# Kernel tuning notes

Measured on AMD Instinct MI355X. Metric: run time of the kernel, lower is better.

The kernel has to match this reference:

```python
import jax, jax.numpy as jnp
import numpy as np

# Core Cutie memory read: L2 affinity with shrinkage/selection + softmax + value readout.
# similarity(n,p) = (-sum_c mk_c(n)^2 * qe_c(p) + 2*sum_c mk_c(n)*qk_c(p)*qe_c(p)
#                   - sum_c qe_c(p)*qk_c(p)^2) * ms(n) / sqrt(CK)
# affinity = softmax over memory dim n; readout = value @ affinity.

NUM_OBJECTS = 3
VALUE_DIM = 512
KEY_DIM = 64
T_MEM, H16, W16 = 16, 30, 54  # 16 memory frames, stride-16 features of 480x864


def setup_inputs() -> dict:
    k = jax.random.key(0)
    k0, k1, k2, k3, k4 = jax.random.split(k, 5)
    B = 1
    N = T_MEM * H16 * W16
    return {
        "memory_key": jax.random.normal(k0, (B, KEY_DIM, N), jnp.float32),
        "memory_shrinkage": jax.random.uniform(k1, (B, 1, N), jnp.float32),
        "key": jax.random.normal(k2, (B, KEY_DIM, H16, W16), jnp.float32),
        "selection": jax.random.uniform(k3, (B, KEY_DIM, H16, W16), jnp.float32),
        "memory_mask_value": jax.random.normal(k4, (B, NUM_OBJECTS, VALUE_DIM, N), jnp.float32),
    }


def reference(memory_key, memory_shrinkage, key, selection, memory_mask_value):
    B, O, CV, N = memory_mask_value.shape
    Ck = memory_key.shape[1]
    H, W = key.shape[-2:]
    P = H * W
    qk = key.reshape(B, Ck, P)        # query keys,      b c p
    qe = selection.reshape(B, Ck, P)  # query selection, b c p
    mk = memory_key                   # memory keys,     b c n
    # anisotropic squared-L2 similarity (XMem/Cutie), shape b n p
    a_sq = jnp.einsum("bcn,bcp->bnp", mk * mk, qe)
    two_ab = 2.0 * jnp.einsum("bcn,bcp->bnp", mk, qk * qe)
    b_sq = jnp.sum(qe * qk * qk, axis=1, keepdims=True)  # b 1 p
    sim = (-a_sq + two_ab - b_sq) * memory_shrinkage[:, 0, :, None]
    sim = sim / jnp.sqrt(jnp.asarray(Ck, sim.dtype))
    affinity = jax.nn.softmax(sim, axis=1)  # softmax over memory elements n
    value = memory_mask_value.reshape(B, O * CV, N)
    mem = jnp.einsum("bvn,bnp->bvp", value, affinity)  # weighted readout
    return mem.reshape(B, O, CV, H, W)
```

## Files before the change

### kernel.cpp

```cpp
#include <hip/hip_runtime.h>
#include <hip/hip_bf16.h>


#define NTOT 25920
#define PTOT 1620
#define VTOT 1536
#define PPAD 1664
#define PPAD2 1792
#define NPAD 25984
#define KF   128
#define SPLITS 6

typedef __hip_bfloat16 bf16;
using frag  = __attribute__((ext_vector_type(8))) short;
using f32x4 = __attribute__((ext_vector_type(4))) float;

#define GLOBAL_AS __attribute__((address_space(1)))
#define LDS_AS    __attribute__((address_space(3)))
__device__ __forceinline__ void async_copy16(void* l, const void* g) {
    __builtin_amdgcn_global_load_lds((const GLOBAL_AS void*)g, (LDS_AS void*)l,
                                     16, 0, 0);
}

#define OFF_FLAG ((size_t)0)
#define OFF_QF   ((size_t)64)
#define OFF_NF   ((size_t)426048)
#define OFF_BSQ  ((size_t)7077952)
#define OFF_MSC  ((size_t)7084608)
#define OFF_SUM  ((size_t)7188544)
#define OFF_ACC  ((size_t)7195200)
#define OFF_ES   ((size_t)17148480)
#define OFF_VALB ((size_t)110045760)
#define NEED_BIG ((size_t)189672000)
#define OFF_PART ((size_t)189672000)
#define NEED_PART ((size_t)249391680)

__global__ void detect_dtype(const unsigned short* __restrict__ mk16,
                             unsigned* __restrict__ flag) {
    int i = threadIdx.x;
    unsigned e = (mk16[2 * i] >> 7) & 0xFFu;
    unsigned long long bad = __ballot(e >= 0x8Fu);
    if (i == 0) *flag = bad ? 1u : 0u;
}

__device__ __forceinline__ float load_in(const void* p, int idx, bool f32) {
    return f32 ? ((const float*)p)[idx]
               : __bfloat162float(((const bf16*)p)[idx]);
}

__global__ __launch_bounds__(256) void prep_q(const void* __restrict__ key,
                                              const void* __restrict__ sel,
                                              bf16* __restrict__ qf,
                                              float* __restrict__ bsq,
                                              float* __restrict__ sums,
                                              const unsigned* __restrict__ flag) {
    const bool f32 = (*flag != 0u);
    int p = blockIdx.x * 256 + threadIdx.x;
    if (p >= PPAD) return;
    float acc = 0.f;
    for (int c = 0; c < 64; ++c) {
        float qk = 0.f, qe = 0.f;
        if (p < PTOT) {
            qk = load_in(key, c * PTOT + p, f32);
            qe = load_in(sel, c * PTOT + p, f32);
        }
        qf[p * KF + c]      = __float2bfloat16(-qe);
        qf[p * KF + 64 + c] = __float2bfloat16(2.f * qk * qe);
        acc += qe * qk * qk;
    }
    bsq[p]  = acc;
    sums[p] = 0.f;
}

__global__ __launch_bounds__(256) void prep_n(const void* __restrict__ mkey,
                                              const void* __restrict__ shr,
                                              bf16* __restrict__ nf,
                                              float* __restrict__ msc,
                                              const unsigned* __restrict__ flag) {
    const bool f32 = (*flag != 0u);
    int n = blockIdx.x * 256 + threadIdx.x;
    if (n >= NPAD) return;
    for (int c = 0; c < 64; ++c) {
        float mk = (n < NTOT) ? load_in(mkey, c * NTOT + n, f32) : 0.f;
        nf[n * KF + c]      = __float2bfloat16(mk * mk);
        nf[n * KF + 64 + c] = __float2bfloat16(mk);
    }
    msc[n] = (n < NTOT) ? load_in(shr, n, f32) * 0.125f : 0.f;
}

__global__ __launch_bounds__(256) void conv_val(const void* __restrict__ val,
                                                bf16* __restrict__ valb,
                                                const unsigned* __restrict__ flag) {
    const bool f32 = (*flag != 0u);
    size_t base = ((size_t)blockIdx.x * 256 + threadIdx.x) * 8;
    if (base >= (size_t)VTOT * NTOT) return;
    if (f32) {
        const float4 v0 = *(const float4*)((const float*)val + base);
        const float4 v1 = *(const float4*)((const float*)val + base + 4);
        bf16 o[8] = {__float2bfloat16(v0.x), __float2bfloat16(v0.y),
                     __float2bfloat16(v0.z), __float2bfloat16(v0.w),
                     __float2bfloat16(v1.x), __float2bfloat16(v1.y),
                     __float2bfloat16(v1.z), __float2bfloat16(v1.w)};
        *(uint4*)(valb + base) = *(const uint4*)o;
    } else {
        *(uint4*)(valb + base) = *(const uint4*)((const bf16*)val + base);
    }
}

#define EST_LD 136
__global__ __launch_bounds__(256) void sim_kernel(const bf16* __restrict__ qf,
                                                  const bf16* __restrict__ nf,
                                                  const float* __restrict__ bsq,
                                                  const float* __restrict__ msc,
                                                  float* __restrict__ sums,
                                                  bf16* __restrict__ es) {
    __shared__ __align__(16) char smem[65536];
    short* As  = (short*)smem;
    short* Bs  = (short*)(smem + 32768);
    short* Est = (short*)smem;

    const int tid = threadIdx.x;
    const int nt = blockIdx.x, pt = blockIdx.y;
    const int p0 = pt * 128, n0 = nt * 128;
    const int w = tid >> 6, lane = tid & 63;

    for (int it = 0; it < 8; ++it) {
        int rb = it * 16 + w * 4;
        int r  = rb + (lane >> 4);
        int cg = (lane & 15) ^ (r & 15);
        async_copy16(&As[rb * KF], qf + (size_t)(p0 + r) * KF + cg * 8);
    }
    for (int it = 0; it < 8; ++it) {
        int rb = it * 16 + w * 4;
        int r  = rb + (lane >> 4);
        int cg = (lane & 15) ^ (r & 15);
        async_copy16(&Bs[rb * KF], nf + (size_t)(n0 + r) * KF + cg * 8);
    }
    __syncthreads();

    const int low = lane & 15, quad = lane >> 4;
    const int wr = w >> 1, wc = w & 1;

    f32x4 acc[4][4] = {};
    for (int kk = 0; kk < 4; ++kk) {
        frag a[4], b[4];
        for (int i = 0; i < 4; ++i) {
            int row = wr * 64 + i * 16 + low;
            a[i] = *(const frag*)&As[row * KF + (((kk * 4 + quad) ^ low) * 8)];
        }
        for (int j = 0; j < 4; ++j) {
            int row = wc * 64 + j * 16 + low;
            b[j] = *(const frag*)&Bs[row * KF + (((kk * 4 + quad) ^ low) * 8)];
        }
        for (int i = 0; i < 4; ++i)
            for (int j = 0; j < 4; ++j)
                acc[i][j] = __builtin_amdgcn_mfma_f32_16x16x32_bf16(a[i], b[j], acc[i][j], 0, 0, 0);
    }

    float msv[4];
    for (int j = 0; j < 4; ++j) msv[j] = msc[n0 + wc * 64 + j * 16 + low];
    __syncthreads();

    for (int i = 0; i < 4; ++i) {
        const int prow = p0 + wr * 64 + i * 16 + quad * 4;
        const float4 bq = *(const float4*)(bsq + prow);
        const float bs[4] = {bq.x, bq.y, bq.z, bq.w};
        for (int r = 0; r < 4; ++r) {
            const int p = prow + r;
            const int rloc = wr * 64 + i * 16 + quad * 4 + r;
            float vsum = 0.f;
            for (int j = 0; j < 4; ++j) {
                const int n = n0 + wc * 64 + j * 16 + low;
                float e = 0.f;
                if (n < NTOT) e = __expf((acc[i][j][r] - bs[r]) * msv[j]);
                vsum += e;
                Est[rloc * EST_LD + wc * 64 + j * 16 + low] = __bfloat16_as_short(__float2bfloat16(e));
            }
            vsum += __shfl_xor(vsum, 1);
            vsum += __shfl_xor(vsum, 2);
            vsum += __shfl_xor(vsum, 4);
            vsum += __shfl_xor(vsum, 8);
            if (p < PTOT && low == 0) atomicAdd(&sums[p], vsum);
        }
    }
    __syncthreads();

    const int row = tid >> 1, half = tid & 1;
    const int p = p0 + row;
    if (p < PTOT) {
        bf16* dst = es + (size_t)p * NTOT + n0 + half * 64;
        const short* src = Est + row * EST_LD + half * 64;
        for (int m = 0; m < 8; ++m) {
            int ng = n0 + half * 64 + m * 8;
            if (ng + 8 <= NTOT)
                *(uint4*)(dst + m * 8) = *(const uint4*)(src + m * 8);
        }
    }
}

__global__ __launch_bounds__(512) void gemm_big(const bf16* __restrict__ val,
                                                const bf16* __restrict__ es,
                                                const float* __restrict__ sums,
                                                float* __restrict__ out,
                                                float* __restrict__ part,
                                                int use_part) {
    __shared__ __align__(16) short As[3][2][128 * 64];
    __shared__ __align__(16) short Bs[2][2][128 * 64];
    const int tid = threadIdx.x;

    const int nwg = (PPAD2 / 256) * (VTOT / 256) * SPLITS;
    const int orig = blockIdx.x;
    const int xcd = orig & 7;
    const int q8 = nwg >> 3, r8 = nwg & 7;
    const int cbase = (xcd < r8) ? xcd * (q8 + 1) : r8 * (q8 + 1) + (xcd - r8) * q8;
    const int wg = cbase + (orig >> 3);
    const int vt = wg % 6;
    const int t2 = wg / 6;
    const int pt = t2 % 7;
    const int s  = t2 / 7;

    const int p0 = pt * 256, v0 = vt * 256;
    const int ks = s * 68;
    const int ke = (ks + 68 < 405) ? ks + 68 : 405;

    const int w = tid >> 6, lane = tid & 63, low = lane & 15, quad = lane >> 4;
    const int wv = w >> 2, wp = w & 3;
    const int rA = lane >> 3;
    const int cgx = (lane & 7) ^ rA;

    auto stageA = [&](int t, int reg, int h) {
        if (t >= ke) return;
        const int k0 = t * 64;
#pragma unroll
        for (int it = 0; it < 2; ++it) {
            int rb = it * 64 + w * 8;
            async_copy16(&As[reg][h][rb * 64],
                         val + (size_t)(v0 + h * 128 + rb + rA) * NTOT + k0 + cgx * 8);
        }
    };
    auto stageB = [&](int t, int h) {
        if (t >= ke) return;
        const int k0 = t * 64, bb = t & 1;
#pragma unroll
        for (int it = 0; it < 2; ++it) {
            int rb = it * 64 + w * 8;
            async_copy16(&Bs[bb][h][rb * 64],
                         es + (size_t)(p0 + h * 128 + rb + rA) * NTOT + k0 + cgx * 8);
        }
    };

    const int hB = wp >> 1;
    const int rB0 = (wp & 1) * 64 + low;
    const int c0 = ((0 * 4 + quad) ^ (low & 7)) * 8;
    const int c1 = ((1 * 4 + quad) ^ (low & 7)) * 8;

    f32x4 acc[8][4] = {};

    int cur = ks % 3;
    int nx1 = (cur + 1 == 3) ? 0 : cur + 1;
    stageA(ks, cur, 0); stageA(ks, cur, 1);
    stageB(ks, 0);      stageB(ks, 1);
    stageA(ks + 1, nx1, 0); stageA(ks + 1, nx1, 1);
    stageB(ks + 1, 0);      stageB(ks + 1, 1);
    asm volatile("s_waitcnt vmcnt(8)" ::: "memory");
    __builtin_amdgcn_s_barrier();

    for (int t = ks; t < ke; ++t) {
        int nx2 = cur + 2; if (nx2 >= 3) nx2 -= 3;
        const short* Ab = As[cur][wv];
        const short* Bb = Bs[t & 1][hB];
        frag bfr[2][4];

#pragma unroll
        for (int q = 0; q < 4; ++q) {
            if (q == 0) {
#pragma unroll
                for (int j = 0; j < 4; ++j) {
                    bfr[0][j] = *(const frag*)&Bb[(rB0 + j * 16) * 64 + c0];
                    bfr[1][j] = *(const frag*)&Bb[(rB0 + j * 16) * 64 + c1];
                }
            }
            frag a00, a01, a10, a11;
            {
                const short* r0 = &Ab[((2 * q) * 16 + low) * 64];
                const short* r1 = &Ab[((2 * q + 1) * 16 + low) * 64];
                a00 = *(const frag*)&r0[c0];
                a01 = *(const frag*)&r0[c1];
                a10 = *(const frag*)&r1[c0];
                a11 = *(const frag*)&r1[c1];
            }
            if (q == 0)      stageA(t + 2, nx2, 0);
            else if (q == 1) stageA(t + 2, nx2, 1);
            else if (q == 2) stageB(t + 2, 0);
            else             stageB(t + 2, 1);

            if (q == 0)
                asm volatile("s_waitcnt lgkmcnt(8)" ::: "memory");
            __builtin_amdgcn_s_barrier();
            asm volatile("s_waitcnt lgkmcnt(0)" ::: "memory");
            __builtin_amdgcn_s_setprio(1);
#pragma unroll
            for (int j = 0; j < 4; ++j) {
                acc[2 * q][j]     = __builtin_amdgcn_mfma_f32_16x16x32_bf16(a00, bfr[0][j], acc[2 * q][j], 0, 0, 0);
                acc[2 * q][j]     = __builtin_amdgcn_mfma_f32_16x16x32_bf16(a01, bfr[1][j], acc[2 * q][j], 0, 0, 0);
                acc[2 * q + 1][j] = __builtin_amdgcn_mfma_f32_16x16x32_bf16(a10, bfr[0][j], acc[2 * q + 1][j], 0, 0, 0);
                acc[2 * q + 1][j] = __builtin_amdgcn_mfma_f32_16x16x32_bf16(a11, bfr[1][j], acc[2 * q + 1][j], 0, 0, 0);
            }
            __builtin_amdgcn_s_setprio(0);
            if (q == 3) {
                if (t + 2 < ke)
                    asm volatile("s_waitcnt vmcnt(8)" ::: "memory");
                else
                    asm volatile("s_waitcnt vmcnt(0)" ::: "memory");
            }
            __builtin_amdgcn_s_barrier();
        }
        cur = nx1; nx1 = nx2;
    }

    float rs[4];
#pragma unroll
    for (int j = 0; j < 4; ++j) {
        const int p = p0 + wp * 64 + j * 16 + low;
        rs[j] = (p < PTOT) ? 1.0f / sums[p] : 0.f;
    }
    if (use_part) {
        float* dst = part + (size_t)s * VTOT * PTOT;
#pragma unroll
        for (int i = 0; i < 8; ++i)
#pragma unroll
            for (int r = 0; r < 4; ++r) {
                const int v = v0 + wv * 128 + i * 16 + quad * 4 + r;
#pragma unroll
                for (int j = 0; j < 4; ++j) {
                    const int p = p0 + wp * 64 + j * 16 + low;
                    if (p < PTOT)
                        dst[(size_t)v * PTOT + p] = acc[i][j][r] * rs[j];
                }
            }
    } else {
#pragma unroll
        for (int i = 0; i < 8; ++i)
#pragma unroll
            for (int r = 0; r < 4; ++r) {
                const int v = v0 + wv * 128 + i * 16 + quad * 4 + r;
#pragma unroll
                for (int j = 0; j < 4; ++j) {
                    const int p = p0 + wp * 64 + j * 16 + low;
                    if (p < PTOT)
                        atomicAdd(&out[(size_t)v * PTOT + p], acc[i][j][r] * rs[j]);
                }
            }
    }
}

__global__ __launch_bounds__(256) void reduce6(const float* __restrict__ part,
                                               float* __restrict__ out) {
    size_t i = ((size_t)blockIdx.x * 256 + threadIdx.x) * 4;
    if (i >= (size_t)VTOT * PTOT) return;
    float4 a = *(const float4*)(part + i);
#pragma unroll
    for (int s = 1; s < SPLITS; ++s) {
        const float4 b = *(const float4*)(part + (size_t)s * VTOT * PTOT + i);
        a.x += b.x; a.y += b.y; a.z += b.z; a.w += b.w;
    }
    *(float4*)(out + i) = a;
}

__global__ __launch_bounds__(256) void gemm_small(const void* __restrict__ val,
                                                  const bf16* __restrict__ es,
                                                  const float* __restrict__ sums,
                                                  float* __restrict__ out,
                                                  const unsigned* __restrict__ flag) {
    __shared__ short As[128 * 64];
    __shared__ short Bs[128 * 64];
    const bool f32 = (*flag != 0u);
    const int tid = threadIdx.x;
    const int pt = blockIdx.x, vt = blockIdx.y, s = blockIdx.z;
    const int p0 = pt * 128, v0 = vt * 128;
    const int ks = s * 51;
    const int ke = (ks + 51 < 405) ? ks + 51 : 405;

    const int w = tid >> 6, lane = tid & 63, low = lane & 15, quad = lane >> 4;
    const int wr = w >> 1, wc = w & 1;

    f32x4 acc[4][4] = {};
    for (int kt = ks; kt < ke; ++kt) {
        const int k0 = kt * 64;
        if (f32) {
            for (int it = 0; it < 8; ++it) {
                int ci = it * 256 + tid, row = ci >> 4, c4 = ci & 15;
                const float4 v = *(const float4*)((const float*)val +
                                  (size_t)(v0 + row) * NTOT + k0 + c4 * 4);
                bf16 o[4] = {__float2bfloat16(v.x), __float2bfloat16(v.y),
                             __float2bfloat16(v.z), __float2bfloat16(v.w)};
                *(uint2*)&As[row * 64 + c4 * 4] = *(const uint2*)o;
            }
        } else {
            for (int it = 0; it < 4; ++it) {
                int ci = it * 256 + tid, row = ci >> 3, c8 = ci & 7;
                ((uint4*)As)[ci] = *(const uint4*)((const bf16*)val +
                                   (size_t)(v0 + row) * NTOT + k0 + c8 * 8);
            }
        }
        for (int it = 0; it < 4; ++it) {
            int ci = it * 256 + tid, row = ci >> 3, c8 = ci & 7;
            ((uint4*)Bs)[ci] = *(const uint4*)(es + (size_t)(p0 + row) * NTOT + k0 + c8 * 8);
        }
        __syncthreads();
        for (int kk = 0; kk < 2; ++kk) {
            frag a[4], b[4];
            for (int i = 0; i < 4; ++i)
                a[i] = *(const frag*)&As[(wr * 64 + i * 16 + low) * 64 + kk * 32 + quad * 8];
            for (int j = 0; j < 4; ++j)
                b[j] = *(const frag*)&Bs[(wc * 64 + j * 16 + low) * 64 + kk * 32 + quad * 8];
            for (int i = 0; i < 4; ++i)
                for (int j = 0; j < 4; ++j)
                    acc[i][j] = __builtin_amdgcn_mfma_f32_16x16x32_bf16(a[i], b[j], acc[i][j], 0, 0, 0);
        }
        __syncthreads();
    }

    float rs[4];
    for (int j = 0; j < 4; ++j) {
        const int p = p0 + wc * 64 + j * 16 + low;
        rs[j] = (p < PTOT) ? 1.0f / sums[p] : 0.f;
    }
    for (int i = 0; i < 4; ++i)
        for (int r = 0; r < 4; ++r) {
            const int v = v0 + wr * 64 + i * 16 + quad * 4 + r;
            for (int j = 0; j < 4; ++j) {
                const int p = p0 + wc * 64 + j * 16 + low;
                if (p < PTOT)
                    atomicAdd(&out[(size_t)v * PTOT + p], acc[i][j][r] * rs[j]);
            }
        }
}

extern "C" void kernel_launch(void* const* d_in, const int* in_sizes, int n_in,
                              void* d_out, int out_size, void* d_ws, size_t ws_size,
                              hipStream_t stream) {
    const void* mkey = d_in[0];
    const void* shr  = d_in[1];
    const void* key  = d_in[2];
    const void* sel  = d_in[3];
    const void* val  = d_in[4];
    float* out = (float*)d_out;

    char* ws = (char*)d_ws;
    unsigned* flag = (unsigned*)(ws + OFF_FLAG);
    bf16*  qf   = (bf16*)(ws + OFF_QF);
    bf16*  nf   = (bf16*)(ws + OFF_NF);
    float* bsq  = (float*)(ws + OFF_BSQ);
    float* msc  = (float*)(ws + OFF_MSC);
    float* sums = (float*)(ws + OFF_SUM);
    bf16*  es   = (bf16*)(ws + OFF_ES);
    bf16*  valb = (bf16*)(ws + OFF_VALB);
    float* part = (float*)(ws + OFF_PART);

    detect_dtype<<<1, 32, 0, stream>>>((const unsigned short*)mkey, flag);
    prep_q<<<(PPAD + 255) / 256, 256, 0, stream>>>(key, sel, qf, bsq, sums, flag);
    prep_n<<<(NPAD + 255) / 256, 256, 0, stream>>>(mkey, shr, nf, msc, flag);
    sim_kernel<<<dim3(NPAD / 128, PPAD / 128), 256, 0, stream>>>(qf, nf, bsq, msc, sums, es);
    if (ws_size >= NEED_BIG) {
        size_t nv = (size_t)VTOT * NTOT;
        conv_val<<<(unsigned)((nv / 8 + 255) / 256), 256, 0, stream>>>(val, valb, flag);
        const int upart = (ws_size >= NEED_PART) ? 1 : 0;
        gemm_big<<<dim3((PPAD2 / 256) * (VTOT / 256) * SPLITS), 512, 0, stream>>>(
            valb, es, sums, out, part, upart);
        if (upart) {
            unsigned nred = (unsigned)(((size_t)VTOT * PTOT / 4 + 255) / 256);
            reduce6<<<nred, 256, 0, stream>>>(part, out);
        }
    } else {
        gemm_small<<<dim3(PPAD / 128, VTOT / 128, 8), 256, 0, stream>>>(val, es, sums, out, flag);
    }
}
```

Before: 628.2 us.

## Loop sim kernel over N chunks with double-buffered key prefetch and partial sums

Each sim_kernel block now keeps its query tile resident in LDS and walks seven consecutive 128-wide memory tiles. The next key tiles are prefetched into a double buffer with async global-to-LDS copies, and the Est staging buffer is kept separate. Per-row softmax denominators are accumulated in registers and written as per-chunk partials, and a new reduce_sums kernel adds them up, replacing the global float atomics. The intent is to cut repeated Q loads, launch granularity and atomic traffic, at the cost of an extra kernel launch, fewer blocks (29x13) and more LDS per block. The p<PTOT guard on es rows was dropped, so padded rows may be written past the es region.

```diff
diff --git a/kernel.cpp b/kernel.cpp
--- a/kernel.cpp
+++ b/kernel.cpp
@@ -10,6 +10,8 @@
 #define NPAD 25984
 #define KF   128
 #define SPLITS 6
+#define NT_CH 7
+#define NCHUNK 29
 
 typedef __hip_bfloat16 bf16;
 using frag  = __attribute__((ext_vector_type(8))) short;
@@ -112,90 +114,139 @@
                                                   const bf16* __restrict__ nf,
                                                   const float* __restrict__ bsq,
                                                   const float* __restrict__ msc,
-                                                  float* __restrict__ sums,
+                                                  float* __restrict__ spart,
                                                   bf16* __restrict__ es) {
-    __shared__ __align__(16) char smem[65536];
-    short* As  = (short*)smem;
-    short* Bs  = (short*)(smem + 32768);
-    short* Est = (short*)smem;
+    __shared__ __align__(16) short Qs[128 * KF];
+    __shared__ __align__(16) short Ns[2][128 * KF];
+    __shared__ __align__(16) short Est[128 * EST_LD];
 
     const int tid = threadIdx.x;
-    const int nt = blockIdx.x, pt = blockIdx.y;
-    const int p0 = pt * 128, n0 = nt * 128;
+    const int ch = blockIdx.x, pt = blockIdx.y;
+    const int p0 = pt * 128;
+    const int nbase = ch * (NT_CH * 128);
     const int w = tid >> 6, lane = tid & 63;
+    const int low = lane & 15, quad = lane >> 4;
+    const int wr = w >> 1, wc = w & 1;
 
     for (int it = 0; it < 8; ++it) {
         int rb = it * 16 + w * 4;
         int r  = rb + (lane >> 4);
         int cg = (lane & 15) ^ (r & 15);
-        async_copy16(&As[rb * KF], qf + (size_t)(p0 + r) * KF + cg * 8);
-    }
-    for (int it = 0; it < 8; ++it) {
-        int rb = it * 16 + w * 4;
-        int r  = rb + (lane >> 4);
-        int cg = (lane & 15) ^ (r & 15);
-        async_copy16(&Bs[rb * KF], nf + (size_t)(n0 + r) * KF + cg * 8);
-    }
-    __syncthreads();
-
-    const int low = lane & 15, quad = lane >> 4;
-    const int wr = w >> 1, wc = w & 1;
-
-    f32x4 acc[4][4] = {};
-    for (int kk = 0; kk < 4; ++kk) {
-        frag a[4], b[4];
+        async_copy16(&Qs[rb * KF], qf + (size_t)(p0 + r) * KF + cg * 8);
+    }
+    auto stageN = [&](int t) {
+        const int n0s = nbase + t * 128;
+        short* dst = Ns[t & 1];
+        for (int it = 0; it < 8; ++it) {
+            int rb = it * 16 + w * 4;
+            int r  = rb + (lane >> 4);
+            int cg = (lane & 15) ^ (r & 15);
+            async_copy16(&dst[rb * KF], nf + (size_t)(n0s + r) * KF + cg * 8);
+        }
+    };
+    stageN(0);
+    stageN(1);
+
+    float vs[4][4] = {};
+
+    for (int t = 0; t < NT_CH; ++t) {
+        const int n0 = nbase + t * 128;
+        const short* Nb = Ns[t & 1];
+
+        asm volatile("s_waitcnt vmcnt(8)" ::: "memory");
+        __builtin_amdgcn_s_barrier();
+
+        f32x4 acc[4][4] = {};
+        __builtin_amdgcn_s_setprio(1);
+        for (int kk = 0; kk < 4; ++kk) {
+            frag a[4], b[4];
+#pragma unroll
+            for (int i = 0; i < 4; ++i) {
+                int row = wr * 64 + i * 16 + low;
+                a[i] = *(const frag*)&Qs[row * KF + (((kk * 4 + quad) ^ low) * 8)];
+            }
+#pragma unroll
+            for (int j = 0; j < 4; ++j) {
+                int row = wc * 64 + j * 16 + low;
+                b[j] = *(const frag*)&Nb[row * KF + (((kk * 4 + quad) ^ low) * 8)];
+            }
+#pragma unroll
+            for (int i = 0; i < 4; ++i)
+#pragma unroll
+                for (int j = 0; j < 4; ++j)
+                    acc[i][j] = __builtin_amdgcn_mfma_f32_16x16x32_bf16(a[i], b[j], acc[i][j], 0, 0, 0);
+        }
+        __builtin_amdgcn_s_setprio(0);
+        asm volatile("s_waitcnt lgkmcnt(0)" ::: "memory");
+        __builtin_amdgcn_s_barrier();
+
+        float msv[4];
+#pragma unroll
+        for (int j = 0; j < 4; ++j) msv[j] = msc[n0 + wc * 64 + j * 16 + low];
+#pragma unroll
         for (int i = 0; i < 4; ++i) {
-            int row = wr * 64 + i * 16 + low;
-            a[i] = *(const frag*)&As[row * KF + (((kk * 4 + quad) ^ low) * 8)];
-        }
-        for (int j = 0; j < 4; ++j) {
-            int row = wc * 64 + j * 16 + low;
-            b[j] = *(const frag*)&Bs[row * KF + (((kk * 4 + quad) ^ low) * 8)];
-        }
-        for (int i = 0; i < 4; ++i)
-            for (int j = 0; j < 4; ++j)
-                acc[i][j] = __builtin_amdgcn_mfma_f32_16x16x32_bf16(a[i], b[j], acc[i][j], 0, 0, 0);
-    }
-
-    float msv[4];
-    for (int j = 0; j < 4; ++j) msv[j] = msc[n0 + wc * 64 + j * 16 + low];
-    __syncthreads();
-
-    for (int i = 0; i < 4; ++i) {
-        const int prow = p0 + wr * 64 + i * 16 + quad * 4;
-        const float4 bq = *(const float4*)(bsq + prow);
-        const float bs[4] = {bq.x, bq.y, bq.z, bq.w};
+            const int prow = p0 + wr * 64 + i * 16 + quad * 4;
+            const float4 bq = *(const float4*)(bsq + prow);
+            const float bsv[4] = {bq.x, bq.y, bq.z, bq.w};
+#pragma unroll
+            for (int r = 0; r < 4; ++r) {
+                const int rloc = wr * 64 + i * 16 + quad * 4 + r;
+                float vsum = 0.f;
+#pragma unroll
+                for (int j = 0; j < 4; ++j) {
+                    const int n = n0 + wc * 64 + j * 16 + low;
+                    float e = 0.f;
+                    if (n < NTOT) e = __expf((acc[i][j][r] - bsv[r]) * msv[j]);
+                    vsum += e;
+                    Est[rloc * EST_LD + wc * 64 + j * 16 + low] =
+                        __bfloat16_as_short(__float2bfloat16(e));
+                }
+                vs[i][r] += vsum;
+            }
+        }
+        asm volatile("s_waitcnt lgkmcnt(0)" ::: "memory");
+        __builtin_amdgcn_s_barrier();
+
+        {
+            const int row = tid >> 1, half = tid & 1;
+            bf16* dst = es + (size_t)(p0 + row) * NTOT + n0 + half * 64;
+            const short* src = Est + row * EST_LD + half * 64;
+#pragma unroll
+            for (int m = 0; m < 8; ++m) {
+                int ng = n0 + half * 64 + m * 8;
+                if (ng + 8 <= NTOT)
+                    *(uint4*)(dst + m * 8) = *(const uint4*)(src + m * 8);
+            }
+        }
+        __builtin_amdgcn_sched_barrier(0);
+        if (t + 2 < NT_CH) stageN(t + 2);
+        __builtin_amdgcn_sched_barrier(0);
+    }
+
+#pragma unroll
+    for (int i = 0; i < 4; ++i)
+#pragma unroll
         for (int r = 0; r < 4; ++r) {
-            const int p = prow + r;
-            const int rloc = wr * 64 + i * 16 + quad * 4 + r;
-            float vsum = 0.f;
-            for (int j = 0; j < 4; ++j) {
-                const int n = n0 + wc * 64 + j * 16 + low;
-                float e = 0.f;
-                if (n < NTOT) e = __expf((acc[i][j][r] - bs[r]) * msv[j]);
-                vsum += e;
-                Est[rloc * EST_LD + wc * 64 + j * 16 + low] = __bfloat16_as_short(__float2bfloat16(e));
-            }
-            vsum += __shfl_xor(vsum, 1);
-            vsum += __shfl_xor(vsum, 2);
-            vsum += __shfl_xor(vsum, 4);
-            vsum += __shfl_xor(vsum, 8);
-            if (p < PTOT && low == 0) atomicAdd(&sums[p], vsum);
-        }
-    }
-    __syncthreads();
-
-    const int row = tid >> 1, half = tid & 1;
-    const int p = p0 + row;
-    if (p < PTOT) {
-        bf16* dst = es + (size_t)p * NTOT + n0 + half * 64;
-        const short* src = Est + row * EST_LD + half * 64;
-        for (int m = 0; m < 8; ++m) {
-            int ng = n0 + half * 64 + m * 8;
-            if (ng + 8 <= NTOT)
-                *(uint4*)(dst + m * 8) = *(const uint4*)(src + m * 8);
-        }
-    }
+            float v = vs[i][r];
+            v += __shfl_xor(v, 1);
+            v += __shfl_xor(v, 2);
+            v += __shfl_xor(v, 4);
+            v += __shfl_xor(v, 8);
+            if (low == 0) {
+                const int p = p0 + wr * 64 + i * 16 + quad * 4 + r;
+                spart[(size_t)(ch * 2 + wc) * PPAD + p] = v;
+            }
+        }
+}
+
+__global__ __launch_bounds__(256) void reduce_sums(const float* __restrict__ spart,
+                                                   float* __restrict__ sums) {
+    int p = blockIdx.x * 256 + threadIdx.x;
+    if (p >= PPAD) return;
+    float a = 0.f;
+#pragma unroll 4
+    for (int k = 0; k < 2 * NCHUNK; ++k) a += spart[(size_t)k * PPAD + p];
+    sums[p] = a;
 }
 
 __global__ __launch_bounds__(512) void gemm_big(const bf16* __restrict__ val,
@@ -454,6 +505,7 @@
     float* bsq  = (float*)(ws + OFF_BSQ);
     float* msc  = (float*)(ws + OFF_MSC);
     float* sums = (float*)(ws + OFF_SUM);
+    float* spart = (float*)(ws + OFF_ACC);
     bf16*  es   = (bf16*)(ws + OFF_ES);
     bf16*  valb = (bf16*)(ws + OFF_VALB);
     float* part = (float*)(ws + OFF_PART);
@@ -461,7 +513,8 @@
     detect_dtype<<<1, 32, 0, stream>>>((const unsigned short*)mkey, flag);
     prep_q<<<(PPAD + 255) / 256, 256, 0, stream>>>(key, sel, qf, bsq, sums, flag);
     prep_n<<<(NPAD + 255) / 256, 256, 0, stream>>>(mkey, shr, nf, msc, flag);
-    sim_kernel<<<dim3(NPAD / 128, PPAD / 128), 256, 0, stream>>>(qf, nf, bsq, msc, sums, es);
+    sim_kernel<<<dim3(NCHUNK, PPAD / 128), 256, 0, stream>>>(qf, nf, bsq, msc, spart, es);
+    reduce_sums<<<(PPAD + 255) / 256, 256, 0, stream>>>(spart, sums);
     if (ws_size >= NEED_BIG) {
         size_t nv = (size_t)VTOT * NTOT;
         conv_val<<<(unsigned)((nv / 8 + 255) / 256), 256, 0, stream>>>(val, valb, flag);
```

After: 576.5 us. -8.2%, faster.
